# Optimization experiments

Measured on AMD Instinct MI355X. Metric: run time of the kernel, lower is better.

The kernel has to match this reference:

```python
import jax, jax.numpy as jnp
import numpy as np


def setup_inputs() -> dict:
    key = jax.random.key(0)
    k1, k2 = jax.random.split(key)
    T, H, E = 16384, 4096, 64
    hidden_states = jax.random.normal(k1, (T, H), dtype=jnp.float32)
    W = jax.random.normal(k2, (E, H), dtype=jnp.float32) * 0.02  # init std=0.02
    b = jnp.zeros((E,), dtype=jnp.float32)
    return {"hidden_states": hidden_states, "W": W, "b": b}


def reference(hidden_states, W, b):
    TOPK = 8
    # Linear: [T, H] @ [H, E] + [E] -> [T, E]
    router_logits = jnp.einsum("th,eh->te", hidden_states, W) + b
    router_probs = jax.nn.sigmoid(router_logits)
    routing_weights, routing_indices = jax.lax.top_k(router_probs, TOPK)
    routing_weights = routing_weights / jnp.sum(routing_weights, axis=-1, keepdims=True)
    return routing_weights, routing_indices, router_probs
```

## Files before the change

kernel.cpp:

```cpp
#include <hip/hip_runtime.h>
#include <math.h>

#define H 4096
#define E 64
#define BK 32
#define BM 64
#define TOPK 8

__global__ __launch_bounds__(256) void router_fused_kernel(
    const float* __restrict__ A, const float* __restrict__ Wm,
    const float* __restrict__ bias, float* __restrict__ weights,
    float* __restrict__ indices, float* __restrict__ probs)
{
    __shared__ float  Alds[BM][BK + 4];
    __shared__ float  Wlds[BK][E];
    __shared__ double Llds[BM][E + 1];

    const int tid  = threadIdx.x;
    const int er   = tid & 15;
    const int rr   = tid >> 4;
    const int lrow = tid >> 3;
    const int seg  = tid & 7;

    const long row0 = (long)blockIdx.x * BM;

    double acc[4][4];
#pragma unroll
    for (int i = 0; i < 4; ++i)
#pragma unroll
        for (int j = 0; j < 4; ++j) acc[i][j] = 0.0;

    float4 pa0 = *(const float4*)(A + (row0 + lrow) * H + seg * 4);
    float4 pa1 = *(const float4*)(A + (row0 + lrow + 32) * H + seg * 4);
    float4 pw0 = *(const float4*)(Wm + (long)lrow * H + seg * 4);
    float4 pw1 = *(const float4*)(Wm + (long)(lrow + 32) * H + seg * 4);

    for (int k0 = 0; k0 < H; k0 += BK) {
        *(float4*)&Alds[lrow][seg * 4]      = pa0;
        *(float4*)&Alds[lrow + 32][seg * 4] = pa1;
        Wlds[seg * 4 + 0][lrow] = pw0.x;
        Wlds[seg * 4 + 1][lrow] = pw0.y;
        Wlds[seg * 4 + 2][lrow] = pw0.z;
        Wlds[seg * 4 + 3][lrow] = pw0.w;
        Wlds[seg * 4 + 0][lrow + 32] = pw1.x;
        Wlds[seg * 4 + 1][lrow + 32] = pw1.y;
        Wlds[seg * 4 + 2][lrow + 32] = pw1.z;
        Wlds[seg * 4 + 3][lrow + 32] = pw1.w;
        __syncthreads();

        if (k0 + BK < H) {
            const int kn = k0 + BK;
            pa0 = *(const float4*)(A + (row0 + lrow) * H + kn + seg * 4);
            pa1 = *(const float4*)(A + (row0 + lrow + 32) * H + kn + seg * 4);
            pw0 = *(const float4*)(Wm + (long)lrow * H + kn + seg * 4);
            pw1 = *(const float4*)(Wm + (long)(lrow + 32) * H + kn + seg * 4);
        }

#pragma unroll
        for (int kk = 0; kk < BK; kk += 4) {
            double a[4][4];
            double w[4][4];
#pragma unroll
            for (int i = 0; i < 4; ++i) {
                const float4 t = *(const float4*)&Alds[rr * 4 + i][kk];
                a[i][0] = (double)t.x; a[i][1] = (double)t.y;
                a[i][2] = (double)t.z; a[i][3] = (double)t.w;
            }
#pragma unroll
            for (int m = 0; m < 4; ++m) {
                const float4 t = *(const float4*)&Wlds[kk + m][er * 4];
                w[m][0] = (double)t.x; w[m][1] = (double)t.y;
                w[m][2] = (double)t.z; w[m][3] = (double)t.w;
            }
#pragma unroll
            for (int m = 0; m < 4; ++m)
#pragma unroll
                for (int i = 0; i < 4; ++i)
#pragma unroll
                    for (int j = 0; j < 4; ++j)
                        acc[i][j] = fma(a[i][m], w[m][j], acc[i][j]);
        }
        __syncthreads();
    }

    const float4 bv = *(const float4*)(bias + er * 4);
    const double bb[4] = {(double)bv.x, (double)bv.y, (double)bv.z, (double)bv.w};
#pragma unroll
    for (int i = 0; i < 4; ++i) {
        float4 o;
        float* op = (float*)&o;
#pragma unroll
        for (int j = 0; j < 4; ++j) {
            const double lg = acc[i][j] + bb[j];
            Llds[rr * 4 + i][er * 4 + j] = lg;
            op[j] = 1.0f / (1.0f + __expf(-(float)lg));
        }
        *(float4*)(probs + (row0 + rr * 4 + i) * E + er * 4) = o;
    }
    __syncthreads();

    if (tid < BM) {
        const int r = tid;
        unsigned long long taken = 0ull;
        float wsel[TOPK];
        int   isel[TOPK];
        float sum = 0.0f;
#pragma unroll
        for (int it = 0; it < TOPK; ++it) {
            double best = -1.0e300;
            int    bi   = 0;
            for (int j = 0; j < E; ++j) {
                if (!((taken >> j) & 1ull)) {
                    const double v = Llds[r][j];
                    if (v > best) { best = v; bi = j; }
                }
            }
            taken |= (1ull << bi);
            const float p = 1.0f / (1.0f + __expf(-(float)best));
            wsel[it] = p;
            isel[it] = bi;
            sum += p;
        }
        const float inv = 1.0f / sum;
#pragma unroll
        for (int it = 0; it < TOPK; ++it) {
            weights[(row0 + r) * TOPK + it] = wsel[it] * inv;
            indices[(row0 + r) * TOPK + it] = (float)isel[it];
        }
    }
}

extern "C" void kernel_launch(void* const* d_in, const int* in_sizes, int n_in,
                              void* d_out, int out_size, void* d_ws, size_t ws_size,
                              hipStream_t stream) {
    const float* A    = (const float*)d_in[0];
    const float* W    = (const float*)d_in[1];
    const float* bias = (const float*)d_in[2];
    const int T = in_sizes[0] / H;

    float* out     = (float*)d_out;
    float* weights = out;
    float* indices = out + (size_t)T * TOPK;
    float* probs   = out + (size_t)T * 2 * TOPK;

    hipLaunchKernelGGL(router_fused_kernel, dim3(T / BM), dim3(256), 0, stream,
                       A, W, bias, weights, indices, probs);
}
```

Measured before the change: 562.4 us.

## Split router into fp32 split-K GEMM, top-k pass, and fp64 recheck of ambiguous rows

Replaces the fused fp64 GEMM kernel with an fp32 split-K GEMM that accumulates into the probs buffer with atomics, using a pre-transposed weight copy. A separate pass applies bias, sigmoid and top-k, and flags rows whose top-9 logit gaps fall below a tolerance. Only the flagged rows are recomputed in fp64 to keep the selection identical to the reference. This removes the costly fp64 FMA throughput bottleneck. In exchange it adds extra launches, a memset, atomics, and a dependence on workspace size for correctness.

```diff
diff --git a/kernel.cpp b/kernel.cpp
--- a/kernel.cpp
+++ b/kernel.cpp
@@ -3,136 +3,205 @@
 
 #define H 4096
 #define E 64
-#define BK 32
-#define BM 64
 #define TOPK 8
-
-__global__ __launch_bounds__(256) void router_fused_kernel(
-    const float* __restrict__ A, const float* __restrict__ Wm,
-    const float* __restrict__ bias, float* __restrict__ weights,
-    float* __restrict__ indices, float* __restrict__ probs)
-{
-    __shared__ float  Alds[BM][BK + 4];
-    __shared__ float  Wlds[BK][E];
-    __shared__ double Llds[BM][E + 1];
-
-    const int tid  = threadIdx.x;
-    const int er   = tid & 15;
-    const int rr   = tid >> 4;
-    const int lrow = tid >> 3;
-    const int seg  = tid & 7;
-
-    const long row0 = (long)blockIdx.x * BM;
-
-    double acc[4][4];
-#pragma unroll
-    for (int i = 0; i < 4; ++i)
-#pragma unroll
-        for (int j = 0; j < 4; ++j) acc[i][j] = 0.0;
-
-    float4 pa0 = *(const float4*)(A + (row0 + lrow) * H + seg * 4);
-    float4 pa1 = *(const float4*)(A + (row0 + lrow + 32) * H + seg * 4);
-    float4 pw0 = *(const float4*)(Wm + (long)lrow * H + seg * 4);
-    float4 pw1 = *(const float4*)(Wm + (long)(lrow + 32) * H + seg * 4);
-
-    for (int k0 = 0; k0 < H; k0 += BK) {
-        *(float4*)&Alds[lrow][seg * 4]      = pa0;
-        *(float4*)&Alds[lrow + 32][seg * 4] = pa1;
-        Wlds[seg * 4 + 0][lrow] = pw0.x;
-        Wlds[seg * 4 + 1][lrow] = pw0.y;
-        Wlds[seg * 4 + 2][lrow] = pw0.z;
-        Wlds[seg * 4 + 3][lrow] = pw0.w;
-        Wlds[seg * 4 + 0][lrow + 32] = pw1.x;
-        Wlds[seg * 4 + 1][lrow + 32] = pw1.y;
-        Wlds[seg * 4 + 2][lrow + 32] = pw1.z;
-        Wlds[seg * 4 + 3][lrow + 32] = pw1.w;
+#define NSLICE 16
+#define KS (H / NSLICE)
+#define TAU 1e-4f
+
+
+__global__ __launch_bounds__(256) void wt_transpose(
+    const float* __restrict__ W, float* __restrict__ Wt)
+{
+    const int t  = blockIdx.x * 256 + threadIdx.x;
+    const int k  = t >> 4;
+    const int e0 = (t & 15) * 4;
+    float4 v;
+    v.x = W[(e0 + 0) * H + k];
+    v.y = W[(e0 + 1) * H + k];
+    v.z = W[(e0 + 2) * H + k];
+    v.w = W[(e0 + 3) * H + k];
+    *(float4*)(Wt + k * E + e0) = v;
+}
+
+__global__ __launch_bounds__(64, 4) void router_gemm(
+    const float* __restrict__ A, const float* __restrict__ Wt,
+    float* __restrict__ logits)
+{
+    const int ks = blockIdx.x & (NSLICE - 1);
+    const int rg = blockIdx.x >> 4;
+    const int k0 = ks * KS;
+    const long row = (long)rg * 64 + threadIdx.x;
+
+    float acc[E];
+#pragma unroll
+    for (int e = 0; e < E; ++e) acc[e] = 0.0f;
+
+    const float* __restrict__ ap = A + row * H + k0;
+    const float* __restrict__ wp = Wt + (long)k0 * E;
+
+#pragma unroll 2
+    for (int k = 0; k < KS; k += 4) {
+        const float4 av = *(const float4*)(ap + k);
+        const float* __restrict__ w0 = wp + (k + 0) * E;
+        const float* __restrict__ w1 = wp + (k + 1) * E;
+        const float* __restrict__ w2 = wp + (k + 2) * E;
+        const float* __restrict__ w3 = wp + (k + 3) * E;
+#pragma unroll
+        for (int e = 0; e < E; ++e) acc[e] = fmaf(av.x, w0[e], acc[e]);
+#pragma unroll
+        for (int e = 0; e < E; ++e) acc[e] = fmaf(av.y, w1[e], acc[e]);
+#pragma unroll
+        for (int e = 0; e < E; ++e) acc[e] = fmaf(av.z, w2[e], acc[e]);
+#pragma unroll
+        for (int e = 0; e < E; ++e) acc[e] = fmaf(av.w, w3[e], acc[e]);
+    }
+
+    float* out = logits + row * E;
+#pragma unroll
+    for (int e = 0; e < E; ++e) atomicAdd(out + e, acc[e]);
+}
+
+__global__ __launch_bounds__(64) void router_topk(
+    float* __restrict__ probs, const float* __restrict__ bias,
+    float* __restrict__ weights, float* __restrict__ indices,
+    int* __restrict__ flagcnt, int* __restrict__ flaglist, int cap)
+{
+    const long row = (long)blockIdx.x * 64 + threadIdx.x;
+    float* pr = probs + row * E;
+
+    float lg[E];
+#pragma unroll
+    for (int e = 0; e < E; e += 4) {
+        const float4 v = *(const float4*)(pr + e);
+        const float4 b = *(const float4*)(bias + e);
+        lg[e + 0] = v.x + b.x;
+        lg[e + 1] = v.y + b.y;
+        lg[e + 2] = v.z + b.z;
+        lg[e + 3] = v.w + b.w;
+    }
+
+#pragma unroll
+    for (int e = 0; e < E; e += 4) {
+        float4 o;
+        o.x = 1.0f / (1.0f + __expf(-lg[e + 0]));
+        o.y = 1.0f / (1.0f + __expf(-lg[e + 1]));
+        o.z = 1.0f / (1.0f + __expf(-lg[e + 2]));
+        o.w = 1.0f / (1.0f + __expf(-lg[e + 3]));
+        *(float4*)(pr + e) = o;
+    }
+
+    unsigned long long taken = 0ull;
+    float sv[TOPK + 1];
+    int   si[TOPK + 1];
+#pragma unroll
+    for (int it = 0; it <= TOPK; ++it) {
+        float best = -3.0e38f;
+        int   bi   = 0;
+#pragma unroll
+        for (int j = 0; j < E; ++j) {
+            const bool ok = !((taken >> j) & 1ull) && (lg[j] > best);
+            best = ok ? lg[j] : best;
+            bi   = ok ? j   : bi;
+        }
+        sv[it] = best;
+        si[it] = bi;
+        taken |= 1ull << bi;
+    }
+
+    float w8[TOPK];
+    float sum = 0.0f;
+#pragma unroll
+    for (int it = 0; it < TOPK; ++it) {
+        w8[it] = 1.0f / (1.0f + __expf(-sv[it]));
+        sum += w8[it];
+    }
+    const float inv = 1.0f / sum;
+#pragma unroll
+    for (int it = 0; it < TOPK; ++it) {
+        weights[row * TOPK + it] = w8[it] * inv;
+        indices[row * TOPK + it] = (float)si[it];
+    }
+
+    bool amb = false;
+#pragma unroll
+    for (int it = 0; it < TOPK; ++it) amb |= (sv[it] - sv[it + 1]) < TAU;
+    if (amb && cap > 0) {
+        const int pos = atomicAdd(flagcnt, 1);
+        if (pos < cap) flaglist[pos] = (int)row;
+    }
+}
+
+__global__ __launch_bounds__(256) void router_recheck(
+    const float* __restrict__ A, const float* __restrict__ W,
+    const float* __restrict__ bias,
+    float* __restrict__ weights, float* __restrict__ indices,
+    const int* __restrict__ flagcnt, const int* __restrict__ flaglist,
+    int cap)
+{
+    __shared__ double part[4][E];
+    __shared__ double lg[E];
+
+    const int e  = threadIdx.x & 63;
+    const int kc = threadIdx.x >> 6;
+
+    int n = *flagcnt;
+    if (n > cap) n = cap;
+
+    for (int f = blockIdx.x; f < n; f += gridDim.x) {
+        const int row = flaglist[f];
+        const float* ar = A + (long)row * H + kc * (H / 4);
+        const float* wr = W + (long)e   * H + kc * (H / 4);
+        double s = 0.0;
+        for (int k = 0; k < H / 4; k += 4) {
+            const float4 av = *(const float4*)(ar + k);
+            const float4 wv = *(const float4*)(wr + k);
+            s = fma((double)av.x, (double)wv.x, s);
+            s = fma((double)av.y, (double)wv.y, s);
+            s = fma((double)av.z, (double)wv.z, s);
+            s = fma((double)av.w, (double)wv.w, s);
+        }
+        part[kc][e] = s;
         __syncthreads();
-
-        if (k0 + BK < H) {
-            const int kn = k0 + BK;
-            pa0 = *(const float4*)(A + (row0 + lrow) * H + kn + seg * 4);
-            pa1 = *(const float4*)(A + (row0 + lrow + 32) * H + kn + seg * 4);
-            pw0 = *(const float4*)(Wm + (long)lrow * H + kn + seg * 4);
-            pw1 = *(const float4*)(Wm + (long)(lrow + 32) * H + kn + seg * 4);
-        }
-
-#pragma unroll
-        for (int kk = 0; kk < BK; kk += 4) {
-            double a[4][4];
-            double w[4][4];
-#pragma unroll
-            for (int i = 0; i < 4; ++i) {
-                const float4 t = *(const float4*)&Alds[rr * 4 + i][kk];
-                a[i][0] = (double)t.x; a[i][1] = (double)t.y;
-                a[i][2] = (double)t.z; a[i][3] = (double)t.w;
+        if (threadIdx.x < E) {
+            const int j = threadIdx.x;
+            lg[j] = ((part[0][j] + part[1][j]) + (part[2][j] + part[3][j]))
+                    + (double)bias[j];
+        }
+        __syncthreads();
+        if (threadIdx.x == 0) {
+            unsigned long long taken = 0ull;
+            float wsel[TOPK];
+            int   isel[TOPK];
+            float psum = 0.0f;
+            for (int it = 0; it < TOPK; ++it) {
+                double best = -1.0e300;
+                int    bi   = 0;
+                for (int j = 0; j < E; ++j) {
+                    if (!((taken >> j) & 1ull)) {
+                        const double v = lg[j];
+                        if (v > best) { best = v; bi = j; }
+                    }
+                }
+                taken |= 1ull << bi;
+                const float p = 1.0f / (1.0f + __expf(-(float)best));
+                wsel[it] = p;
+                isel[it] = bi;
+                psum += p;
             }
-#pragma unroll
-            for (int m = 0; m < 4; ++m) {
-                const float4 t = *(const float4*)&Wlds[kk + m][er * 4];
-                w[m][0] = (double)t.x; w[m][1] = (double)t.y;
-                w[m][2] = (double)t.z; w[m][3] = (double)t.w;
+            const float inv = 1.0f / psum;
+            for (int it = 0; it < TOPK; ++it) {
+                weights[(long)row * TOPK + it] = wsel[it] * inv;
+                indices[(long)row * TOPK + it] = (float)isel[it];
             }
-#pragma unroll
-            for (int m = 0; m < 4; ++m)
-#pragma unroll
-                for (int i = 0; i < 4; ++i)
-#pragma unroll
-                    for (int j = 0; j < 4; ++j)
-                        acc[i][j] = fma(a[i][m], w[m][j], acc[i][j]);
         }
         __syncthreads();
-    }
-
-    const float4 bv = *(const float4*)(bias + er * 4);
-    const double bb[4] = {(double)bv.x, (double)bv.y, (double)bv.z, (double)bv.w};
-#pragma unroll
-    for (int i = 0; i < 4; ++i) {
-        float4 o;
-        float* op = (float*)&o;
-#pragma unroll
-        for (int j = 0; j < 4; ++j) {
-            const double lg = acc[i][j] + bb[j];
-            Llds[rr * 4 + i][er * 4 + j] = lg;
-            op[j] = 1.0f / (1.0f + __expf(-(float)lg));
-        }
-        *(float4*)(probs + (row0 + rr * 4 + i) * E + er * 4) = o;
-    }
-    __syncthreads();
-
-    if (tid < BM) {
-        const int r = tid;
-        unsigned long long taken = 0ull;
-        float wsel[TOPK];
-        int   isel[TOPK];
-        float sum = 0.0f;
-#pragma unroll
-        for (int it = 0; it < TOPK; ++it) {
-            double best = -1.0e300;
-            int    bi   = 0;
-            for (int j = 0; j < E; ++j) {
-                if (!((taken >> j) & 1ull)) {
-                    const double v = Llds[r][j];
-                    if (v > best) { best = v; bi = j; }
-                }
-            }
-            taken |= (1ull << bi);
-            const float p = 1.0f / (1.0f + __expf(-(float)best));
-            wsel[it] = p;
-            isel[it] = bi;
-            sum += p;
-        }
-        const float inv = 1.0f / sum;
-#pragma unroll
-        for (int it = 0; it < TOPK; ++it) {
-            weights[(row0 + r) * TOPK + it] = wsel[it] * inv;
-            indices[(row0 + r) * TOPK + it] = (float)isel[it];
-        }
     }
 }
 
 extern "C" void kernel_launch(void* const* d_in, const int* in_sizes, int n_in,
                               void* d_out, int out_size, void* d_ws, size_t ws_size,
-                              hipStream_t stream) {
+                              hipStream_t stream)
+{
     const float* A    = (const float*)d_in[0];
     const float* W    = (const float*)d_in[1];
     const float* bias = (const float*)d_in[2];
@@ -143,6 +212,21 @@
     float* indices = out + (size_t)T * TOPK;
     float* probs   = out + (size_t)T * 2 * TOPK;
 
-    hipLaunchKernelGGL(router_fused_kernel, dim3(T / BM), dim3(256), 0, stream,
-                       A, W, bias, weights, indices, probs);
-}
+    float* Wt = (float*)d_ws;
+    const size_t WT_BYTES = (size_t)H * E * sizeof(float);
+    int* flagcnt  = (int*)((char*)d_ws + WT_BYTES);
+    int* flaglist = flagcnt + 4;
+    long cap_l = ((long)ws_size - (long)WT_BYTES - 16) / 4;
+    int  cap   = cap_l < 0 ? 0 : (cap_l > T ? T : (int)cap_l);
+
+    hipMemsetAsync(probs, 0, (size_t)T * E * sizeof(float), stream);
+    if (cap > 0) hipMemsetAsync(flagcnt, 0, sizeof(int), stream);
+
+    wt_transpose<<<(H * E / 4) / 256, 256, 0, stream>>>(W, Wt);
+    router_gemm<<<(T / 64) * NSLICE, 64, 0, stream>>>(A, Wt, probs);
+    router_topk<<<T / 64, 64, 0, stream>>>(probs, bias, weights, indices,
+                                           flagcnt, flaglist, cap);
+    if (cap > 0)
+        router_recheck<<<256, 256, 0, stream>>>(A, W, bias, weights, indices,
+                                                flagcnt, flaglist, cap);
+}
```

Result: slower. 1.290 ms (+129.4%).
